# Kernel optimization log

Measured on AMD Instinct MI355X. Metric: run time of the kernel, lower is better.

The kernel has to match this reference:

```python
import jax, jax.numpy as jnp
import numpy as np

MB, SEQ, EMBDIM, N_TOKENS = 8, 2048, 64, 8192


def setup_inputs() -> dict:
    key = jax.random.key(0)
    k1, k2 = jax.random.split(key)
    X = jax.random.normal(k1, (MB, SEQ, EMBDIM), dtype=jnp.float32)
    weight = jax.random.normal(k2, (N_TOKENS, EMBDIM), dtype=jnp.float32)
    return {"X": X, "weight": weight}


def reference(X, weight):
    adotb = jnp.einsum("bse,ne->bsn", X, weight)            # [mb, seq, n_tokens]
    adota = jnp.sum(X * X, axis=-1, keepdims=True)           # [mb, seq, 1]
    bdotb = jnp.sum(weight * weight, axis=-1)                # [n_tokens]
    dist = adota - 2.0 * adotb + bdotb                       # [mb, seq, n_tokens]
    return jnp.argmin(dist, axis=-1)                         # [mb, seq] int indices
```

## Files before the change

kernel.cpp:

```cpp
#include <hip/hip_runtime.h>
#include <math.h>

#define EMB     64
#define NTOK    8192
#define NQ      16384
#define TPB     256
#define CSPLIT  4
#define CRANGE  (NTOK / CSPLIT)
#define BQ      128
#define TILE_C  128
#define NT      (CRANGE / TILE_C)
#define TCH     (TILE_C * EMB)
#define NXBLK   (NQ / BQ)

typedef _Float16 half8 __attribute__((ext_vector_type(8)));
typedef float    f32x4 __attribute__((ext_vector_type(4)));

__device__ __forceinline__ void gl2lds16(const _Float16* g, _Float16* l) {
    __builtin_amdgcn_global_load_lds(
        (const __attribute__((address_space(1))) unsigned int*)g,
        (__attribute__((address_space(3))) unsigned int*)l, 16, 0, 0);
}

__device__ __forceinline__ unsigned long long pack_di(float d, int idx) {
    unsigned int u = __float_as_uint(d);
    unsigned int m = (u & 0x80000000u) ? ~u : (u | 0x80000000u);
    return ((unsigned long long)m << 32) | (unsigned int)idx;
}

__global__ void prep_kernel(const float* __restrict__ W,
                            _Float16* __restrict__ Wh, _Float16* __restrict__ Wl,
                            float* __restrict__ ynorm,
                            unsigned long long* __restrict__ packed,
                            int* __restrict__ cnt) {
    const int gtid = blockIdx.x * blockDim.x + threadIdx.x;
    if (gtid < NQ)    packed[gtid] = ~0ull;
    if (gtid < NXBLK) cnt[gtid] = 0;

    const int c   = gtid >> 3;
    const int seg = gtid & 7;
    const float* wp = W + (size_t)c * EMB + seg * 8;
    float4 v0 = *(const float4*)wp;
    float4 v1 = *(const float4*)(wp + 4);
    float xv[8] = {v0.x, v0.y, v0.z, v0.w, v1.x, v1.y, v1.z, v1.w};
    half8 h, l;
    float s8 = 0.f;
#pragma unroll
    for (int j = 0; j < 8; ++j) {
        _Float16 hh = (_Float16)xv[j];
        h[j] = hh;
        l[j] = (_Float16)(xv[j] - (float)hh);
        s8 = fmaf(xv[j], xv[j], s8);
    }
    const int g = c >> 4, r = c & 15, kb = seg >> 2, lq = seg & 3;
    const size_t u = (size_t)g * 128 + kb * 64 + lq * 16 + r;
    *(half8*)(Wh + u * 8) = h;
    *(half8*)(Wl + u * 8) = l;

    s8 += __shfl_xor(s8, 1, 64);
    s8 += __shfl_xor(s8, 2, 64);
    s8 += __shfl_xor(s8, 4, 64);
    if (seg == 0) ynorm[c] = s8;
}

__global__ __launch_bounds__(TPB, 3) void vq_mfma_kernel(
    const float* __restrict__ X,
    const _Float16* __restrict__ Wh, const _Float16* __restrict__ Wl,
    const float* __restrict__ ynorm,
    unsigned long long* __restrict__ packed,
    int* __restrict__ cnt, int* __restrict__ out)
{
    __shared__ __align__(16) _Float16 LdsH0[TCH];
    __shared__ __align__(16) _Float16 LdsH1[TCH];
    __shared__ __align__(16) _Float16 LdsL0[TCH];
    __shared__ __align__(16) _Float16 LdsL1[TCH];
    __shared__ __align__(16) float    Lyn[CRANGE];
    __shared__ float RedV[2][BQ];
    __shared__ int   RedI[2][BQ];
    __shared__ int   fin;

    const int t    = threadIdx.x;
    const int lane = t & 63;
    const int wid  = t >> 6;
    const int wq   = wid & 1;
    const int wy   = wid >> 1;
    const int l15  = lane & 15;
    const int lq   = lane >> 4;

    const int bx     = blockIdx.x;
    const int qblk   = bx * BQ;
    const int qbase  = qblk + wq * 64;
    const int cbase0 = blockIdx.y * CRANGE;

    {
        const size_t gsbase = (size_t)(cbase0 >> 4) * 1024;
#pragma unroll
        for (int i = 0; i < 4; ++i) {
            const int jw = i * 256 + wid * 64;
            gl2lds16(Wh + gsbase + (size_t)(jw + lane) * 8, LdsH0 + (size_t)jw * 8);
            gl2lds16(Wl + gsbase + (size_t)(jw + lane) * 8, LdsL0 + (size_t)jw * 8);
        }
    }

    for (int u = t; u < CRANGE / 4; u += TPB)
        ((float4*)Lyn)[u] = ((const float4*)(ynorm + cbase0))[u];

    half8 ah[4][2], al[4][2];
#pragma unroll
    for (int mt = 0; mt < 4; ++mt) {
#pragma unroll
        for (int kb = 0; kb < 2; ++kb) {
            const float* xp = X + (size_t)(qbase + mt * 16 + l15) * EMB + kb * 32 + lq * 8;
            float4 v0 = *(const float4*)xp;
            float4 v1 = *(const float4*)(xp + 4);
            float xv[8] = {v0.x, v0.y, v0.z, v0.w, v1.x, v1.y, v1.z, v1.w};
            half8 h, l;
#pragma unroll
            for (int j = 0; j < 8; ++j) {
                _Float16 hh = (_Float16)xv[j];
                float    rr = xv[j] - (float)hh;
                h[j] = (_Float16)(-2.0f * (float)hh);
                l[j] = (_Float16)(-2.0f * rr);
            }
            ah[mt][kb] = h;
            al[mt][kb] = l;
        }
    }

    float minv[4][4];
    int   mini[4][4];
#pragma unroll
    for (int mt = 0; mt < 4; ++mt)
#pragma unroll
        for (int r = 0; r < 4; ++r) { minv[mt][r] = INFINITY; mini[mt][r] = 0; }

    __syncthreads();

    int cur = 0;
    for (int tt = 0; tt < NT; ++tt) {
        if (tt + 1 < NT) {
            const size_t gsbase = (size_t)((cbase0 + (tt + 1) * TILE_C) >> 4) * 1024;
            _Float16* dH = (cur ^ 1) ? LdsH1 : LdsH0;
            _Float16* dL = (cur ^ 1) ? LdsL1 : LdsL0;
#pragma unroll
            for (int i = 0; i < 4; ++i) {
                const int jw = i * 256 + wid * 64;
                gl2lds16(Wh + gsbase + (size_t)(jw + lane) * 8, dH + (size_t)jw * 8);
                gl2lds16(Wl + gsbase + (size_t)(jw + lane) * 8, dL + (size_t)jw * 8);
            }
        }

        const _Float16* LH = cur ? LdsH1 : LdsH0;
        const _Float16* LL = cur ? LdsL1 : LdsL0;
        const int c0 = tt * TILE_C;
#pragma unroll
        for (int ct = 0; ct < 4; ++ct) {
            const int chunk0 = (wy * 4 + ct) * 128 + lane;
            const int ccol   = wy * 64 + ct * 16;
            const float yn   = Lyn[c0 + ccol + l15];
            const f32x4 yn4  = {yn, yn, yn, yn};
            half8 bh0 = *(const half8*)(LH + (size_t)chunk0 * 8);
            half8 bl0 = *(const half8*)(LL + (size_t)chunk0 * 8);
            half8 bh1 = *(const half8*)(LH + (size_t)(chunk0 + 64) * 8);
            half8 bl1 = *(const half8*)(LL + (size_t)(chunk0 + 64) * 8);
            f32x4 acc[4];
#pragma unroll
            for (int mt = 0; mt < 4; ++mt) {
                f32x4 a = __builtin_amdgcn_mfma_f32_16x16x32_f16(al[mt][0], bh0, yn4, 0, 0, 0);
                a = __builtin_amdgcn_mfma_f32_16x16x32_f16(ah[mt][0], bl0, a, 0, 0, 0);
                a = __builtin_amdgcn_mfma_f32_16x16x32_f16(ah[mt][0], bh0, a, 0, 0, 0);
                a = __builtin_amdgcn_mfma_f32_16x16x32_f16(al[mt][1], bh1, a, 0, 0, 0);
                a = __builtin_amdgcn_mfma_f32_16x16x32_f16(ah[mt][1], bl1, a, 0, 0, 0);
                a = __builtin_amdgcn_mfma_f32_16x16x32_f16(ah[mt][1], bh1, a, 0, 0, 0);
                acc[mt] = a;
            }
            const int cidx = cbase0 + c0 + ccol + l15;
#pragma unroll
            for (int mt = 0; mt < 4; ++mt) {
#pragma unroll
                for (int r = 0; r < 4; ++r) {
                    float s = acc[mt][r];
                    if (s < minv[mt][r]) { minv[mt][r] = s; mini[mt][r] = cidx; }
                }
            }
        }

        asm volatile("s_waitcnt vmcnt(0)" ::: "memory");
        asm volatile("s_waitcnt lgkmcnt(0)" ::: "memory");
        __builtin_amdgcn_s_barrier();
        cur ^= 1;
    }

#pragma unroll
    for (int mt = 0; mt < 4; ++mt) {
#pragma unroll
        for (int r = 0; r < 4; ++r) {
            float v = minv[mt][r];
            int   i = mini[mt][r];
#pragma unroll
            for (int m = 1; m <= 8; m <<= 1) {
                float ov = __shfl_xor(v, m, 64);
                int   oi = __shfl_xor(i, m, 64);
                if (ov < v || (ov == v && oi < i)) { v = ov; i = oi; }
            }
            if (l15 == 0) {
                int qoff = wq * 64 + mt * 16 + lq * 4 + r;
                RedV[wy][qoff] = v;
                RedI[wy][qoff] = i;
            }
        }
    }
    __syncthreads();

    if (t < BQ) {
        float v0 = RedV[0][t]; int i0 = RedI[0][t];
        float v1 = RedV[1][t]; int i1 = RedI[1][t];
        if (v1 < v0 || (v1 == v0 && i1 < i0)) { v0 = v1; i0 = i1; }
        atomicMin(&packed[qblk + t], pack_di(v0, i0));
    }
    asm volatile("s_waitcnt vmcnt(0)" ::: "memory");
    __syncthreads();
    if (t == 0) fin = (atomicAdd(&cnt[bx], 1) == CSPLIT - 1);
    __syncthreads();
    if (fin && t < BQ) {
        unsigned long long v = atomicMin(&packed[qblk + t], ~0ull);
        out[qblk + t] = (int)(unsigned int)(v & 0xFFFFFFFFu);
    }
}

extern "C" void kernel_launch(void* const* d_in, const int* in_sizes, int n_in,
                              void* d_out, int out_size, void* d_ws, size_t ws_size,
                              hipStream_t stream) {
    const float* X = (const float*)d_in[0];
    const float* W = (const float*)d_in[1];

    _Float16* Wh    = (_Float16*)d_ws;
    _Float16* Wl    = Wh + (size_t)NTOK * EMB;
    float*    ynorm = (float*)(Wl + (size_t)NTOK * EMB);
    unsigned long long* packed = (unsigned long long*)(ynorm + NTOK);
    int*      cnt   = (int*)(packed + NQ);
    int*      out   = (int*)d_out;

    prep_kernel<<<(NTOK * 8) / TPB, TPB, 0, stream>>>(W, Wh, Wl, ynorm, packed, cnt);
    dim3 grid(NXBLK, CSPLIT);
    vq_mfma_kernel<<<grid, TPB, 0, stream>>>(X, Wh, Wl, ynorm, packed, cnt, out);
}
```

Baseline: 108.2 us.

## Switch distance MFMA from 16x16x32 to 32x32x16 tiles with matching weight layout

Replaces the 16x16x32 f16 MFMA tiling with 32x32x16 MFMAs, changing the prepacked weight layout, the A-fragment loading and the per-lane min tracking and reduction to suit the 32x32 output layout. Larger MFMA tiles are meant to raise operand reuse per LDS read and cut instruction overhead. They also double the per-lane accumulator and min/index state, so launch bounds drop from 3 to 2 blocks per SM to leave room for the extra registers. This lowers occupancy and adds a longer cross-lane shuffle reduction.

```diff
diff --git a/kernel.cpp b/kernel.cpp
--- a/kernel.cpp
+++ b/kernel.cpp
@@ -13,8 +13,8 @@
 #define TCH     (TILE_C * EMB)
 #define NXBLK   (NQ / BQ)
 
-typedef _Float16 half8 __attribute__((ext_vector_type(8)));
-typedef float    f32x4 __attribute__((ext_vector_type(4)));
+typedef _Float16 half8  __attribute__((ext_vector_type(8)));
+typedef float    f32x16 __attribute__((ext_vector_type(16)));
 
 __device__ __forceinline__ void gl2lds16(const _Float16* g, _Float16* l) {
     __builtin_amdgcn_global_load_lds(
@@ -52,8 +52,8 @@
         l[j] = (_Float16)(xv[j] - (float)hh);
         s8 = fmaf(xv[j], xv[j], s8);
     }
-    const int g = c >> 4, r = c & 15, kb = seg >> 2, lq = seg & 3;
-    const size_t u = (size_t)g * 128 + kb * 64 + lq * 16 + r;
+    const size_t u = (size_t)(c >> 5) * 256 + (seg >> 1) * 64
+                   + (seg & 1) * 32 + (c & 31);
     *(half8*)(Wh + u * 8) = h;
     *(half8*)(Wl + u * 8) = l;
 
@@ -63,7 +63,7 @@
     if (seg == 0) ynorm[c] = s8;
 }
 
-__global__ __launch_bounds__(TPB, 3) void vq_mfma_kernel(
+__global__ __launch_bounds__(TPB, 2) void vq_mfma_kernel(
     const float* __restrict__ X,
     const _Float16* __restrict__ Wh, const _Float16* __restrict__ Wl,
     const float* __restrict__ ynorm,
@@ -84,8 +84,8 @@
     const int wid  = t >> 6;
     const int wq   = wid & 1;
     const int wy   = wid >> 1;
-    const int l15  = lane & 15;
-    const int lq   = lane >> 4;
+    const int l31  = lane & 31;
+    const int lh   = lane >> 5;
 
     const int bx     = blockIdx.x;
     const int qblk   = bx * BQ;
@@ -93,7 +93,7 @@
     const int cbase0 = blockIdx.y * CRANGE;
 
     {
-        const size_t gsbase = (size_t)(cbase0 >> 4) * 1024;
+        const size_t gsbase = (size_t)cbase0 * 64;
 #pragma unroll
         for (int i = 0; i < 4; ++i) {
             const int jw = i * 256 + wid * 64;
@@ -105,12 +105,13 @@
     for (int u = t; u < CRANGE / 4; u += TPB)
         ((float4*)Lyn)[u] = ((const float4*)(ynorm + cbase0))[u];
 
-    half8 ah[4][2], al[4][2];
-#pragma unroll
-    for (int mt = 0; mt < 4; ++mt) {
-#pragma unroll
-        for (int kb = 0; kb < 2; ++kb) {
-            const float* xp = X + (size_t)(qbase + mt * 16 + l15) * EMB + kb * 32 + lq * 8;
+    half8 ah[2][4], al[2][4];
+#pragma unroll
+    for (int mtile = 0; mtile < 2; ++mtile) {
+#pragma unroll
+        for (int ks = 0; ks < 4; ++ks) {
+            const float* xp = X + (size_t)(qbase + mtile * 32 + l31) * EMB
+                            + ks * 16 + lh * 8;
             float4 v0 = *(const float4*)xp;
             float4 v1 = *(const float4*)(xp + 4);
             float xv[8] = {v0.x, v0.y, v0.z, v0.w, v1.x, v1.y, v1.z, v1.w};
@@ -122,24 +123,26 @@
                 h[j] = (_Float16)(-2.0f * (float)hh);
                 l[j] = (_Float16)(-2.0f * rr);
             }
-            ah[mt][kb] = h;
-            al[mt][kb] = l;
-        }
-    }
-
-    float minv[4][4];
-    int   mini[4][4];
-#pragma unroll
-    for (int mt = 0; mt < 4; ++mt)
-#pragma unroll
-        for (int r = 0; r < 4; ++r) { minv[mt][r] = INFINITY; mini[mt][r] = 0; }
+            ah[mtile][ks] = h;
+            al[mtile][ks] = l;
+        }
+    }
+
+    float minv[2][16];
+    int   mini[2][16];
+#pragma unroll
+    for (int mtile = 0; mtile < 2; ++mtile)
+#pragma unroll
+        for (int r = 0; r < 16; ++r) { minv[mtile][r] = INFINITY; mini[mtile][r] = 0; }
 
     __syncthreads();
 
     int cur = 0;
     for (int tt = 0; tt < NT; ++tt) {
+        const int cb = cbase0 + tt * TILE_C;
+
         if (tt + 1 < NT) {
-            const size_t gsbase = (size_t)((cbase0 + (tt + 1) * TILE_C) >> 4) * 1024;
+            const size_t gsbase = (size_t)(cb + TILE_C) * 64;
             _Float16* dH = (cur ^ 1) ? LdsH1 : LdsH0;
             _Float16* dL = (cur ^ 1) ? LdsL1 : LdsL0;
 #pragma unroll
@@ -154,33 +157,33 @@
         const _Float16* LL = cur ? LdsL1 : LdsL0;
         const int c0 = tt * TILE_C;
 #pragma unroll
-        for (int ct = 0; ct < 4; ++ct) {
-            const int chunk0 = (wy * 4 + ct) * 128 + lane;
-            const int ccol   = wy * 64 + ct * 16;
-            const float yn   = Lyn[c0 + ccol + l15];
-            const f32x4 yn4  = {yn, yn, yn, yn};
-            half8 bh0 = *(const half8*)(LH + (size_t)chunk0 * 8);
-            half8 bl0 = *(const half8*)(LL + (size_t)chunk0 * 8);
-            half8 bh1 = *(const half8*)(LH + (size_t)(chunk0 + 64) * 8);
-            half8 bl1 = *(const half8*)(LL + (size_t)(chunk0 + 64) * 8);
-            f32x4 acc[4];
-#pragma unroll
-            for (int mt = 0; mt < 4; ++mt) {
-                f32x4 a = __builtin_amdgcn_mfma_f32_16x16x32_f16(al[mt][0], bh0, yn4, 0, 0, 0);
-                a = __builtin_amdgcn_mfma_f32_16x16x32_f16(ah[mt][0], bl0, a, 0, 0, 0);
-                a = __builtin_amdgcn_mfma_f32_16x16x32_f16(ah[mt][0], bh0, a, 0, 0, 0);
-                a = __builtin_amdgcn_mfma_f32_16x16x32_f16(al[mt][1], bh1, a, 0, 0, 0);
-                a = __builtin_amdgcn_mfma_f32_16x16x32_f16(ah[mt][1], bl1, a, 0, 0, 0);
-                a = __builtin_amdgcn_mfma_f32_16x16x32_f16(ah[mt][1], bh1, a, 0, 0, 0);
-                acc[mt] = a;
-            }
-            const int cidx = cbase0 + c0 + ccol + l15;
-#pragma unroll
-            for (int mt = 0; mt < 4; ++mt) {
-#pragma unroll
-                for (int r = 0; r < 4; ++r) {
-                    float s = acc[mt][r];
-                    if (s < minv[mt][r]) { minv[mt][r] = s; mini[mt][r] = cidx; }
+        for (int ctile = 0; ctile < 2; ++ctile) {
+            const int cbase = (wy * 2 + ctile) * 256 + lane;
+            half8 bh[4], bl[4];
+#pragma unroll
+            for (int ks = 0; ks < 4; ++ks) {
+                bh[ks] = *(const half8*)(LH + (size_t)(cbase + ks * 64) * 8);
+                bl[ks] = *(const half8*)(LL + (size_t)(cbase + ks * 64) * 8);
+            }
+            const int   ccol = wy * 64 + ctile * 32;
+            const float yn   = Lyn[c0 + ccol + l31];
+            const int   cidx = cb + ccol + l31;
+            f32x16 yn16;
+#pragma unroll
+            for (int r = 0; r < 16; ++r) yn16[r] = yn;
+#pragma unroll
+            for (int mtile = 0; mtile < 2; ++mtile) {
+                f32x16 a = yn16;
+#pragma unroll
+                for (int ks = 0; ks < 4; ++ks) {
+                    a = __builtin_amdgcn_mfma_f32_32x32x16_f16(al[mtile][ks], bh[ks], a, 0, 0, 0);
+                    a = __builtin_amdgcn_mfma_f32_32x32x16_f16(ah[mtile][ks], bl[ks], a, 0, 0, 0);
+                    a = __builtin_amdgcn_mfma_f32_32x32x16_f16(ah[mtile][ks], bh[ks], a, 0, 0, 0);
+                }
+#pragma unroll
+                for (int r = 0; r < 16; ++r) {
+                    float s = a[r];
+                    if (s < minv[mtile][r]) { minv[mtile][r] = s; mini[mtile][r] = cidx; }
                 }
             }
         }
@@ -192,19 +195,19 @@
     }
 
 #pragma unroll
-    for (int mt = 0; mt < 4; ++mt) {
-#pragma unroll
-        for (int r = 0; r < 4; ++r) {
-            float v = minv[mt][r];
-            int   i = mini[mt][r];
-#pragma unroll
-            for (int m = 1; m <= 8; m <<= 1) {
+    for (int mtile = 0; mtile < 2; ++mtile) {
+#pragma unroll
+        for (int r = 0; r < 16; ++r) {
+            float v = minv[mtile][r];
+            int   i = mini[mtile][r];
+#pragma unroll
+            for (int m = 1; m <= 16; m <<= 1) {
                 float ov = __shfl_xor(v, m, 64);
                 int   oi = __shfl_xor(i, m, 64);
                 if (ov < v || (ov == v && oi < i)) { v = ov; i = oi; }
             }
-            if (l15 == 0) {
-                int qoff = wq * 64 + mt * 16 + lq * 4 + r;
+            if (l31 == 0) {
+                int qoff = wq * 64 + mtile * 32 + (r & 3) + 8 * (r >> 2) + 4 * lh;
                 RedV[wy][qoff] = v;
                 RedI[wy][qoff] = i;
             }
```

Result: slower. 119.3 us (+10.3%).
